# Performance work log

Measured on AMD Instinct MI355X. Metric: run time of the kernel, lower is better.

## Reference

```python
import jax, jax.numpy as jnp
import numpy as np

B, L, C, F, K = 16, 512, 384, 384, 3
MAX_DUR = 8
MEL_MAX = L * MAX_DUR  # fixed expanded length (padded/masked)
PAD = (K - 1) // 2


def conv1d(x, w, b):
    # x: [B, T, C] ; w: [F, C, K] ; 'same' padding as Conv1d(padding=(K-1)//2)
    y = jax.lax.conv_general_dilated(x.transpose(0, 2, 1), w, (1,), [(PAD, PAD)],
                                     dimension_numbers=('NCH', 'OIH', 'NCH'))
    return y.transpose(0, 2, 1) + b


def layernorm(x, g, b, eps=1e-5):
    mu = jnp.mean(x, axis=-1, keepdims=True)
    var = jnp.mean(jnp.square(x - mu), axis=-1, keepdims=True)
    return (x - mu) * jax.lax.rsqrt(var + eps) * g + b


def predictor(x, w1, b1, g1, be1, w2, b2, g2, be2, wl, bl):
    # Conv -> ReLU -> LN -> (Dropout=id) -> Conv -> ReLU -> LN -> Linear(F,1)
    h = layernorm(jax.nn.relu(conv1d(x, w1, b1)), g1, be1)
    h = layernorm(jax.nn.relu(conv1d(h, w2, b2)), g2, be2)
    return h @ wl + bl  # [B, T, 1]


def length_regulate(x, dur):
    # gather/repeat-interleave form of the dense one-hot alignment matmul
    cum = jnp.cumsum(dur, axis=-1)                       # [B, L]
    t = jnp.arange(MEL_MAX)                              # [T]
    idx = (t[None, :, None] >= cum[:, None, :]).sum(-1)  # [B, T] frame->phoneme
    idx = jnp.minimum(idx, x.shape[1] - 1)
    out = jnp.take_along_axis(x, idx[..., None], axis=1)  # [B, T, C]
    mask = (t[None, :] < cum[:, -1:]).astype(x.dtype)      # zero padded frames
    return out * mask[..., None]


def _pred_params(key, prefix):
    ks = jax.random.split(key, 4)
    s = 0.05
    return {
        f'{prefix}_w1': jax.random.normal(ks[0], (F, C, K), jnp.float32) * s,
        f'{prefix}_b1': jnp.zeros((F,), jnp.float32),
        f'{prefix}_g1': jnp.ones((F,), jnp.float32),
        f'{prefix}_be1': jnp.zeros((F,), jnp.float32),
        f'{prefix}_w2': jax.random.normal(ks[1], (F, F, K), jnp.float32) * s,
        f'{prefix}_b2': jnp.zeros((F,), jnp.float32),
        f'{prefix}_g2': jnp.ones((F,), jnp.float32),
        f'{prefix}_be2': jnp.zeros((F,), jnp.float32),
        f'{prefix}_wl': jax.random.normal(ks[2], (F, 1), jnp.float32) * s,
        f'{prefix}_bl': jnp.zeros((1,), jnp.float32),
    }


def setup_inputs() -> dict:
    key = jax.random.key(0)
    kx, kd, k1, k2, k3 = jax.random.split(key, 5)
    inp = {'x': jax.random.normal(kx, (B, L, C), jnp.float32)}
    inp.update(_pred_params(k1, 'dp'))
    inp.update(_pred_params(k2, 'pp'))
    inp.update(_pred_params(k3, 'ep'))
    inp['dur'] = jax.random.randint(kd, (B, L), 0, MAX_DUR, jnp.int32)
    return inp


def reference(x,
              dp_w1, dp_b1, dp_g1, dp_be1, dp_w2, dp_b2, dp_g2, dp_be2, dp_wl, dp_bl,
              pp_w1, pp_b1, pp_g1, pp_be1, pp_w2, pp_b2, pp_g2, pp_be2, pp_wl, pp_bl,
              ep_w1, ep_b1, ep_g1, ep_be1, ep_w2, ep_b2, ep_g2, ep_be2, ep_wl, ep_bl,
              dur):
    durations = predictor(x, dp_w1, dp_b1, dp_g1, dp_be1, dp_w2, dp_b2, dp_g2, dp_be2, dp_wl, dp_bl)
    expanded = length_regulate(x, dur)                    # [B, MEL_MAX, C]
    pitches = predictor(expanded, pp_w1, pp_b1, pp_g1, pp_be1, pp_w2, pp_b2, pp_g2, pp_be2, pp_wl, pp_bl)
    out = expanded + pitches
    energies = predictor(out, ep_w1, ep_b1, ep_g1, ep_be1, ep_w2, ep_b2, ep_g2, ep_be2, ep_wl, ep_bl)
    out = out + energies
    return (out, durations, pitches, energies)
```

## Files before the change

### kernel.cpp

```cpp
#include <hip/hip_runtime.h>
#include <stdint.h>
#include <stdio.h>

#define BB   16
#define LL   512
#define CC   384
#define FF   384
#define KW   3
#define MEL  4096
#define KKT  (CC*KW)

#define O_OUT 0
#define N_OUT (BB*MEL*CC)
#define O_DUR (N_OUT)
#define O_PIT (O_DUR + BB*LL)
#define O_EN  (O_PIT + BB*MEL)

using bf16x8 = __attribute__((ext_vector_type(8))) short;
using f32x4  = __attribute__((ext_vector_type(4))) float;

__device__ __forceinline__ unsigned short f2bf(float v) {
    union { float f; unsigned int u; } cv; cv.f = v;
    unsigned int u = cv.u;
    u += 0x7FFFu + ((u >> 16) & 1u);
    return (unsigned short)(u >> 16);
}
__device__ __forceinline__ float bf2f(unsigned short u) {
    union { unsigned int u; float f; } cv; cv.u = ((unsigned int)u) << 16; return cv.f;
}

__device__ __forceinline__ void gld_lds16(const unsigned short* gp, unsigned short* lp) {
    __builtin_amdgcn_global_load_lds(
        (const __attribute__((address_space(1))) unsigned int*)gp,
        (__attribute__((address_space(3))) unsigned int*)lp, 16, 0, 0);
}

__global__ void wtrans_kernel(const float* __restrict__ w, unsigned short* __restrict__ wt2) {
    int i = blockIdx.x * 256 + threadIdx.x;
    if (i >= FF * KKT) return;
    const int t = i / 24576;
    const int r = i - t * 24576;
    const int c = r >> 3;
    const int e = r & 7;
    const int q = c / 384;
    const int bn = c - q * 384;
    const int kk = t * 64 + q * 8 + e;
    const int k = kk / CC;
    const int ch = kk - k * CC;
    wt2[i] = f2bf(w[(size_t)bn * KKT + ch * KW + k]);
}

__global__ void convert_x_kernel(const float* __restrict__ x, unsigned short* __restrict__ o) {
    int i = blockIdx.x * 256 + threadIdx.x;
    if (i >= BB * LL * CC) return;
    int b = i / (LL * CC);
    int r = i - b * (LL * CC);
    int t = r / CC;
    int c = r - t * CC;
    o[((size_t)b * (LL + 2) + t + 1) * CC + c] = f2bf(x[i]);
}

__global__ void zpad_kernel(unsigned short* __restrict__ buf, int T) {
    int b = blockIdx.x >> 1;
    int w = blockIdx.x & 1;
    size_t row = (size_t)b * (T + 2) + (w ? (T + 1) : 0);
    buf[row * CC + threadIdx.x] = 0;
}

template<int T, bool FL>
__global__ __launch_bounds__(512)
void conv_ln_kernel(const unsigned short* __restrict__ inb,
                    const unsigned short* __restrict__ wt2,
                    const float* __restrict__ bias,
                    const float* __restrict__ g,
                    const float* __restrict__ be,
                    unsigned short* __restrict__ outb,
                    const float* __restrict__ wl,
                    const float* __restrict__ bl,
                    float* __restrict__ op) {
    __shared__ __align__(16) unsigned short LDS[4][8192];

    constexpr int NT = KKT / 64;
    const int m0 = blockIdx.x * 128;
    const int b  = m0 / T;
    const int t0 = m0 - b * T;
    const int tid  = threadIdx.x;
    const int lane = tid & 63;
    const int wv   = tid >> 6;
    const int wr   = wv >> 2;
    const int wc   = wv & 3;
    const int q0   = lane >> 4;
    const int l15  = lane & 15;

    const int rowS = tid >> 3;
    const int gch  = (tid & 7) ^ (rowS & 7);
    const unsigned short* srcA0 =
        inb + ((size_t)b * (T + 2) + t0 + rowS) * CC + gch * 8;
    const unsigned short* srcA1 =
        inb + ((size_t)b * (T + 2) + t0 + 64 + rowS) * CC + gch * 8;
    const unsigned short* wtb0 = wt2 + (size_t)((q0)     * 384 + wc * 96 + l15) * 8;
    const unsigned short* wtb1 = wt2 + (size_t)((4 + q0) * 384 + wc * 96 + l15) * 8;

    f32x4 acc[4][6] = {};
    bf16x8 bA[6], bB[6];

    auto stageA = [&](int bi, int t) {
        const int off = t * 64;
        gld_lds16(srcA0 + off, &LDS[bi][wv * 512]);
        gld_lds16(srcA1 + off, &LDS[bi][4096 + wv * 512]);
    };
    auto loadB0 = [&](int t) {
        const unsigned short* p = wtb0 + (size_t)t * 24576;
        #pragma unroll
        for (int j = 0; j < 6; ++j) bA[j] = *(const bf16x8*)(p + j * 128);
    };
    auto loadB1 = [&](int t) {
        const unsigned short* p = wtb1 + (size_t)t * 24576;
        #pragma unroll
        for (int j = 0; j < 6; ++j) bB[j] = *(const bf16x8*)(p + j * 128);
    };
    auto computeK = [&](int bi, int kkq, const bf16x8* br) {
        bf16x8 af[4];
        const int ca = kkq ^ (lane & 7);
        #pragma unroll
        for (int i = 0; i < 4; ++i) {
            const int ar = wr * 64 + i * 16 + l15;
            af[i] = *(const bf16x8*)(&LDS[bi][ar * 64 + ca * 8]);
        }
        __builtin_amdgcn_s_setprio(1);
        #pragma unroll
        for (int i = 0; i < 4; ++i)
            #pragma unroll
            for (int j = 0; j < 6; ++j)
                acc[i][j] = __builtin_amdgcn_mfma_f32_16x16x32_bf16(
                    af[i], br[j], acc[i][j], 0, 0, 0);
        __builtin_amdgcn_s_setprio(0);
    };

    stageA(0, 0);
    loadB0(0);
    stageA(1, 1);
    asm volatile("s_waitcnt vmcnt(8)" ::: "memory");

    for (int t = 0; t < NT; ++t) {
        __builtin_amdgcn_s_barrier();
        asm volatile("" ::: "memory");
        loadB1(t);
        stageA((t + 2) & 3, (t + 2 > NT - 1) ? NT - 1 : t + 2);
        asm volatile("s_waitcnt vmcnt(8)" ::: "memory");
        computeK(t & 3, q0, bA);
        loadB0((t + 1 > NT - 1) ? NT - 1 : t + 1);
        asm volatile("s_waitcnt vmcnt(8)" ::: "memory");
        computeK(t & 3, 4 + q0, bB);
    }
    asm volatile("s_waitcnt vmcnt(0)" ::: "memory");
    __syncthreads();

    const int colb = wc * 96 + (lane & 15);
    float b6[6];
    #pragma unroll
    for (int j = 0; j < 6; ++j) b6[j] = bias[colb + j * 16];
    #pragma unroll
    for (int i = 0; i < 4; ++i)
        #pragma unroll
        for (int j = 0; j < 6; ++j)
            #pragma unroll
            for (int r = 0; r < 4; ++r) {
                float v = acc[i][j][r] + b6[j];
                acc[i][j][r] = v > 0.f ? v : 0.f;
            }

    float S1[4][4], S2[4][4];
    #pragma unroll
    for (int i = 0; i < 4; ++i)
        #pragma unroll
        for (int r = 0; r < 4; ++r) {
            float s = 0.f, s2 = 0.f;
            #pragma unroll
            for (int j = 0; j < 6; ++j) { const float v = acc[i][j][r]; s += v; s2 += v * v; }
            #pragma unroll
            for (int m = 1; m <= 8; m <<= 1) { s += __shfl_xor(s, m); s2 += __shfl_xor(s2, m); }
            S1[i][r] = s; S2[i][r] = s2;
        }

    float2* red = (float2*)&LDS[0][0];
    if ((lane & 15) == 0) {
        const int q = lane >> 4;
        #pragma unroll
        for (int i = 0; i < 4; ++i)
            #pragma unroll
            for (int r = 0; r < 4; ++r)
                red[(wr * 64 + i * 16 + q * 4 + r) * 4 + wc] = make_float2(S1[i][r], S2[i][r]);
    }
    __syncthreads();

    float g6[6], be6[6];
    #pragma unroll
    for (int j = 0; j < 6; ++j) { g6[j] = g[colb + j * 16]; be6[j] = be[colb + j * 16]; }

    if (!FL) {
        #pragma unroll
        for (int i = 0; i < 4; ++i)
            #pragma unroll
            for (int r = 0; r < 4; ++r) {
                const int row = wr * 64 + i * 16 + (lane >> 4) * 4 + r;
                const float2 p0 = red[row * 4 + 0], p1 = red[row * 4 + 1];
                const float2 p2 = red[row * 4 + 2], p3 = red[row * 4 + 3];
                const float S = p0.x + p1.x + p2.x + p3.x;
                const float Q = p0.y + p1.y + p2.y + p3.y;
                const float mu = S * (1.f / 384.f);
                const float rs = rsqrtf(Q * (1.f / 384.f) - mu * mu + 1e-5f);
                unsigned short* qp = outb + ((size_t)b * (T + 2) + t0 + row + 1) * CC + colb;
                #pragma unroll
                for (int j = 0; j < 6; ++j)
                    qp[j * 16] = f2bf((acc[i][j][r] - mu) * rs * g6[j] + be6[j]);
            }
    } else {
        float wl6[6];
        #pragma unroll
        for (int j = 0; j < 6; ++j) wl6[j] = wl[colb + j * 16];
        float* redl = (float*)&LDS[1][0];
        #pragma unroll
        for (int i = 0; i < 4; ++i)
            #pragma unroll
            for (int r = 0; r < 4; ++r) {
                const int row = wr * 64 + i * 16 + (lane >> 4) * 4 + r;
                const float2 p0 = red[row * 4 + 0], p1 = red[row * 4 + 1];
                const float2 p2 = red[row * 4 + 2], p3 = red[row * 4 + 3];
                const float S = p0.x + p1.x + p2.x + p3.x;
                const float Q = p0.y + p1.y + p2.y + p3.y;
                const float mu = S * (1.f / 384.f);
                const float rs = rsqrtf(Q * (1.f / 384.f) - mu * mu + 1e-5f);
                float sl = 0.f;
                #pragma unroll
                for (int j = 0; j < 6; ++j)
                    sl += ((acc[i][j][r] - mu) * rs * g6[j] + be6[j]) * wl6[j];
                #pragma unroll
                for (int m = 1; m <= 8; m <<= 1) sl += __shfl_xor(sl, m);
                if ((lane & 15) == 0) redl[row * 4 + wc] = sl;
            }
        __syncthreads();
        if (tid < 128)
            op[m0 + tid] = redl[tid * 4] + redl[tid * 4 + 1] +
                           redl[tid * 4 + 2] + redl[tid * 4 + 3] + bl[0];
    }
}

__global__ void cumsum_kernel(const int* __restrict__ dur, int* __restrict__ cum) {
    __shared__ int s[LL];
    const int b = blockIdx.x, t = threadIdx.x;
    s[t] = dur[b * LL + t];
    __syncthreads();
    for (int off = 1; off < LL; off <<= 1) {
        int v = (t >= off) ? s[t - off] : 0;
        __syncthreads();
        s[t] += v;
        __syncthreads();
    }
    cum[b * LL + t] = s[t];
}

__global__ void idx_kernel(const int* __restrict__ cum, int* __restrict__ idxm) {
    const int i = blockIdx.x * 256 + threadIdx.x;
    if (i >= BB * MEL) return;
    const int b = i / MEL, t = i - b * MEL;
    const int* cb = cum + b * LL;
    const int total = cb[LL - 1];
    int lo = 0, hi = LL;
    while (lo < hi) {
        const int mid = (lo + hi) >> 1;
        if (cb[mid] <= t) lo = mid + 1; else hi = mid;
    }
    int id = lo > LL - 1 ? LL - 1 : lo;
    idxm[i] = (t < total) ? id : -1;
}

__global__ void gather_kernel(const float* __restrict__ x, const int* __restrict__ idxm,
                              unsigned short* __restrict__ bb0) {
    const int i = blockIdx.x * 256 + threadIdx.x;
    const int row = i / 96;
    const int c4  = (i - row * 96) * 4;
    const int b = row >> 12, t = row & (MEL - 1);
    const int id = idxm[row];
    float4 v = make_float4(0.f, 0.f, 0.f, 0.f);
    if (id >= 0) v = *(const float4*)(x + ((size_t)b * LL + id) * CC + c4);
    uint2 pk;
    pk.x = (unsigned int)f2bf(v.x) | ((unsigned int)f2bf(v.y) << 16);
    pk.y = (unsigned int)f2bf(v.z) | ((unsigned int)f2bf(v.w) << 16);
    *(uint2*)(bb0 + ((size_t)b * (MEL + 2) + t + 1) * CC + c4) = pk;
}

__global__ void addp_kernel(const unsigned short* __restrict__ bb0,
                            const float* __restrict__ pv,
                            unsigned short* __restrict__ be0) {
    const int i = blockIdx.x * 256 + threadIdx.x;
    const int row = i / 48;
    const int c8  = (i - row * 48) * 8;
    const int b = row >> 12, t = row & (MEL - 1);
    const float p = pv[row];
    const size_t o = ((size_t)b * (MEL + 2) + t + 1) * CC + c8;
    const uint4 in = *(const uint4*)(bb0 + o);
    uint4 ot;
    const unsigned int w[4] = {in.x, in.y, in.z, in.w};
    unsigned int r[4];
    #pragma unroll
    for (int k = 0; k < 4; ++k) {
        const float lo = bf2f((unsigned short)w[k]) + p;
        const float hi = bf2f((unsigned short)(w[k] >> 16)) + p;
        r[k] = (unsigned int)f2bf(lo) | ((unsigned int)f2bf(hi) << 16);
    }
    ot.x = r[0]; ot.y = r[1]; ot.z = r[2]; ot.w = r[3];
    *(uint4*)(be0 + o) = ot;
}

__global__ void final_kernel(const float* __restrict__ x, const int* __restrict__ idxm,
                             const float* __restrict__ pv, const float* __restrict__ ev,
                             float* __restrict__ out0) {
    const int i = blockIdx.x * 256 + threadIdx.x;
    const int row = i / 96;
    const int c4  = (i - row * 96) * 4;
    const int b = row >> 12;
    const int id = idxm[row];
    const float add = pv[row] + ev[row];
    float4 v = make_float4(0.f, 0.f, 0.f, 0.f);
    if (id >= 0) v = *(const float4*)(x + ((size_t)b * LL + id) * CC + c4);
    v.x += add; v.y += add; v.z += add; v.w += add;
    *(float4*)(out0 + (size_t)row * CC + c4) = v;
}

extern "C" void kernel_launch(void* const* d_in, const int* in_sizes, int n_in,
                              void* d_out, int out_size, void* d_ws, size_t ws_size,
                              hipStream_t stream) {
    const float* x = (const float*)d_in[0];
    const float* P[30];
    for (int i = 0; i < 30; ++i) P[i] = (const float*)d_in[1 + i];
    const int* dur = (const int*)d_in[31];
    float* out = (float*)d_out;

    char* ws = (char*)d_ws;
    const size_t WTT_ELEMS = (size_t)FF * KKT;
    const size_t WTT_BYTES = WTT_ELEMS * 2;
    unsigned short* wtt[6];
    for (int i = 0; i < 6; ++i) wtt[i] = (unsigned short*)(ws + i * WTT_BYTES);
    int* cum  = (int*)(ws + 5308416);
    int* idxm = (int*)(ws + 5341184);
    unsigned short* sb0 = (unsigned short*)(ws + 5603328);
    unsigned short* h1s = (unsigned short*)(ws + 11919360);
    unsigned short* bb0 = (unsigned short*)(ws + 18235392);
    unsigned short* h1p = (unsigned short*)(ws + 68616192);
    unsigned short* be0 = (unsigned short*)(ws + 118996992);
    const size_t need = 169377792;
    if (ws_size < need)
        fprintf(stderr, "kernel_launch: ws too small: %zu < %zu\n", ws_size, need);

    const float *dp_w1=P[0], *dp_b1=P[1], *dp_g1=P[2], *dp_be1=P[3], *dp_w2=P[4],
                *dp_b2=P[5], *dp_g2=P[6], *dp_be2=P[7], *dp_wl=P[8], *dp_bl=P[9];
    const float *pp_w1=P[10], *pp_b1=P[11], *pp_g1=P[12], *pp_be1=P[13], *pp_w2=P[14],
                *pp_b2=P[15], *pp_g2=P[16], *pp_be2=P[17], *pp_wl=P[18], *pp_bl=P[19];
    const float *ep_w1=P[20], *ep_b1=P[21], *ep_g1=P[22], *ep_be1=P[23], *ep_w2=P[24],
                *ep_b2=P[25], *ep_g2=P[26], *ep_be2=P[27], *ep_wl=P[28], *ep_bl=P[29];

    const int wtg = (int)((WTT_ELEMS + 255) / 256);
    wtrans_kernel<<<wtg, 256, 0, stream>>>(dp_w1, wtt[0]);
    wtrans_kernel<<<wtg, 256, 0, stream>>>(dp_w2, wtt[1]);
    wtrans_kernel<<<wtg, 256, 0, stream>>>(pp_w1, wtt[2]);
    wtrans_kernel<<<wtg, 256, 0, stream>>>(pp_w2, wtt[3]);
    wtrans_kernel<<<wtg, 256, 0, stream>>>(ep_w1, wtt[4]);
    wtrans_kernel<<<wtg, 256, 0, stream>>>(ep_w2, wtt[5]);

    convert_x_kernel<<<(BB * LL * CC + 255) / 256, 256, 0, stream>>>(x, sb0);
    zpad_kernel<<<BB * 2, CC, 0, stream>>>(sb0, LL);
    zpad_kernel<<<BB * 2, CC, 0, stream>>>(h1s, LL);
    zpad_kernel<<<BB * 2, CC, 0, stream>>>(bb0, MEL);
    zpad_kernel<<<BB * 2, CC, 0, stream>>>(h1p, MEL);
    zpad_kernel<<<BB * 2, CC, 0, stream>>>(be0, MEL);

    cumsum_kernel<<<BB, LL, 0, stream>>>(dur, cum);
    idx_kernel<<<(BB * MEL + 255) / 256, 256, 0, stream>>>(cum, idxm);

    conv_ln_kernel<LL, false><<<BB * LL / 128, 512, 0, stream>>>(
        sb0, wtt[0], dp_b1, dp_g1, dp_be1, h1s, nullptr, nullptr, nullptr);
    conv_ln_kernel<LL, true><<<BB * LL / 128, 512, 0, stream>>>(
        h1s, wtt[1], dp_b2, dp_g2, dp_be2, nullptr, dp_wl, dp_bl, out + O_DUR);

    gather_kernel<<<BB * MEL * 96 / 256, 256, 0, stream>>>(x, idxm, bb0);

    conv_ln_kernel<MEL, false><<<BB * MEL / 128, 512, 0, stream>>>(
        bb0, wtt[2], pp_b1, pp_g1, pp_be1, h1p, nullptr, nullptr, nullptr);
    conv_ln_kernel<MEL, true><<<BB * MEL / 128, 512, 0, stream>>>(
        h1p, wtt[3], pp_b2, pp_g2, pp_be2, nullptr, pp_wl, pp_bl, out + O_PIT);

    addp_kernel<<<BB * MEL * 48 / 256, 256, 0, stream>>>(bb0, out + O_PIT, be0);

    conv_ln_kernel<MEL, false><<<BB * MEL / 128, 512, 0, stream>>>(
        be0, wtt[4], ep_b1, ep_g1, ep_be1, h1p, nullptr, nullptr, nullptr);
    conv_ln_kernel<MEL, true><<<BB * MEL / 128, 512, 0, stream>>>(
        h1p, wtt[5], ep_b2, ep_g2, ep_be2, nullptr, ep_wl, ep_bl, out + O_EN);

    final_kernel<<<BB * MEL * 96 / 256, 256, 0, stream>>>(
        x, idxm, out + O_PIT, out + O_EN, out + O_OUT);
}
```

Baseline: 449.9 us.

## Repartition conv GEMM warps to full-row 128x48 tiles and unroll pipeline by two

Each of the 8 waves now covers all 128 rows of the block against 48 output columns, where before a 2x4 wave grid gave each wave 64 rows by 96 columns. The aim is to halve per-wave B-fragment global loads and register pressure. The cost is twice the LDS A-fragment reads per wave and an 8-way LayerNorm reduction instead of 4-way. The main loop is also manually unrolled by two with retuned vmcnt waits to overlap staging with MFMA. This unrolling assumes NT is even and relies on carefully counted wait thresholds.

```diff
diff --git a/kernel.cpp b/kernel.cpp
--- a/kernel.cpp
+++ b/kernel.cpp
@@ -87,8 +87,6 @@
     const int tid  = threadIdx.x;
     const int lane = tid & 63;
     const int wv   = tid >> 6;
-    const int wr   = wv >> 2;
-    const int wc   = wv & 3;
     const int q0   = lane >> 4;
     const int l15  = lane & 15;
 
@@ -98,11 +96,11 @@
         inb + ((size_t)b * (T + 2) + t0 + rowS) * CC + gch * 8;
     const unsigned short* srcA1 =
         inb + ((size_t)b * (T + 2) + t0 + 64 + rowS) * CC + gch * 8;
-    const unsigned short* wtb0 = wt2 + (size_t)((q0)     * 384 + wc * 96 + l15) * 8;
-    const unsigned short* wtb1 = wt2 + (size_t)((4 + q0) * 384 + wc * 96 + l15) * 8;
-
-    f32x4 acc[4][6] = {};
-    bf16x8 bA[6], bB[6];
+    const unsigned short* wtb0 = wt2 + (size_t)((q0)     * 384 + wv * 48 + l15) * 8;
+    const unsigned short* wtb1 = wt2 + (size_t)((4 + q0) * 384 + wv * 48 + l15) * 8;
+
+    f32x4 acc[8][3] = {};
+    bf16x8 bA[3], bB[3];
 
     auto stageA = [&](int bi, int t) {
         const int off = t * 64;
@@ -112,137 +110,144 @@
     auto loadB0 = [&](int t) {
         const unsigned short* p = wtb0 + (size_t)t * 24576;
         #pragma unroll
-        for (int j = 0; j < 6; ++j) bA[j] = *(const bf16x8*)(p + j * 128);
+        for (int j = 0; j < 3; ++j) bA[j] = *(const bf16x8*)(p + j * 128);
     };
     auto loadB1 = [&](int t) {
         const unsigned short* p = wtb1 + (size_t)t * 24576;
         #pragma unroll
-        for (int j = 0; j < 6; ++j) bB[j] = *(const bf16x8*)(p + j * 128);
+        for (int j = 0; j < 3; ++j) bB[j] = *(const bf16x8*)(p + j * 128);
     };
     auto computeK = [&](int bi, int kkq, const bf16x8* br) {
-        bf16x8 af[4];
-        const int ca = kkq ^ (lane & 7);
-        #pragma unroll
-        for (int i = 0; i < 4; ++i) {
-            const int ar = wr * 64 + i * 16 + l15;
+        bf16x8 af[8];
+        const int ca = kkq ^ (l15 & 7);
+        #pragma unroll
+        for (int i = 0; i < 8; ++i) {
+            const int ar = i * 16 + l15;
             af[i] = *(const bf16x8*)(&LDS[bi][ar * 64 + ca * 8]);
         }
         __builtin_amdgcn_s_setprio(1);
         #pragma unroll
-        for (int i = 0; i < 4; ++i)
-            #pragma unroll
-            for (int j = 0; j < 6; ++j)
+        for (int i = 0; i < 8; ++i)
+            #pragma unroll
+            for (int j = 0; j < 3; ++j)
                 acc[i][j] = __builtin_amdgcn_mfma_f32_16x16x32_bf16(
                     af[i], br[j], acc[i][j], 0, 0, 0);
         __builtin_amdgcn_s_setprio(0);
     };
 
     stageA(0, 0);
+    stageA(1, 1);
     loadB0(0);
-    stageA(1, 1);
-    asm volatile("s_waitcnt vmcnt(8)" ::: "memory");
-
-    for (int t = 0; t < NT; ++t) {
+    asm volatile("s_waitcnt vmcnt(3)" ::: "memory");
+
+    #pragma unroll 1
+    for (int t = 0; t < NT; t += 2) {
         __builtin_amdgcn_s_barrier();
         asm volatile("" ::: "memory");
+        stageA((t + 2) & 3, (t + 2 > NT - 1) ? NT - 1 : t + 2);
         loadB1(t);
-        stageA((t + 2) & 3, (t + 2 > NT - 1) ? NT - 1 : t + 2);
-        asm volatile("s_waitcnt vmcnt(8)" ::: "memory");
+        asm volatile("s_waitcnt vmcnt(5)" ::: "memory");
         computeK(t & 3, q0, bA);
-        loadB0((t + 1 > NT - 1) ? NT - 1 : t + 1);
-        asm volatile("s_waitcnt vmcnt(8)" ::: "memory");
+        loadB0(t + 1);
+        asm volatile("s_waitcnt vmcnt(3)" ::: "memory");
         computeK(t & 3, 4 + q0, bB);
+        stageA((t + 3) & 3, (t + 3 > NT - 1) ? NT - 1 : t + 3);
+        loadB1(t + 1);
+        asm volatile("s_waitcnt vmcnt(5)" ::: "memory");
+        computeK((t + 1) & 3, q0, bA);
+        loadB0((t + 2 > NT - 1) ? NT - 1 : t + 2);
+        asm volatile("s_waitcnt vmcnt(5)" ::: "memory");
+        computeK((t + 1) & 3, 4 + q0, bB);
+        asm volatile("s_waitcnt vmcnt(3)" ::: "memory");
     }
     asm volatile("s_waitcnt vmcnt(0)" ::: "memory");
     __syncthreads();
 
-    const int colb = wc * 96 + (lane & 15);
-    float b6[6];
+    const int colb = wv * 48 + l15;
+    float b3[3];
     #pragma unroll
-    for (int j = 0; j < 6; ++j) b6[j] = bias[colb + j * 16];
+    for (int j = 0; j < 3; ++j) b3[j] = bias[colb + j * 16];
     #pragma unroll
-    for (int i = 0; i < 4; ++i)
-        #pragma unroll
-        for (int j = 0; j < 6; ++j)
+    for (int i = 0; i < 8; ++i)
+        #pragma unroll
+        for (int j = 0; j < 3; ++j)
             #pragma unroll
             for (int r = 0; r < 4; ++r) {
-                float v = acc[i][j][r] + b6[j];
+                float v = acc[i][j][r] + b3[j];
                 acc[i][j][r] = v > 0.f ? v : 0.f;
             }
 
-    float S1[4][4], S2[4][4];
+    float2* red = (float2*)&LDS[0][0];
     #pragma unroll
-    for (int i = 0; i < 4; ++i)
+    for (int i = 0; i < 8; ++i)
         #pragma unroll
         for (int r = 0; r < 4; ++r) {
             float s = 0.f, s2 = 0.f;
             #pragma unroll
-            for (int j = 0; j < 6; ++j) { const float v = acc[i][j][r]; s += v; s2 += v * v; }
+            for (int j = 0; j < 3; ++j) { const float v = acc[i][j][r]; s += v; s2 += v * v; }
             #pragma unroll
             for (int m = 1; m <= 8; m <<= 1) { s += __shfl_xor(s, m); s2 += __shfl_xor(s2, m); }
-            S1[i][r] = s; S2[i][r] = s2;
+            if (l15 == 0)
+                red[(i * 16 + q0 * 4 + r) * 8 + wv] = make_float2(s, s2);
         }
-
-    float2* red = (float2*)&LDS[0][0];
-    if ((lane & 15) == 0) {
-        const int q = lane >> 4;
-        #pragma unroll
-        for (int i = 0; i < 4; ++i)
-            #pragma unroll
-            for (int r = 0; r < 4; ++r)
-                red[(wr * 64 + i * 16 + q * 4 + r) * 4 + wc] = make_float2(S1[i][r], S2[i][r]);
-    }
     __syncthreads();
 
-    float g6[6], be6[6];
+    float g3[3], be3[3];
     #pragma unroll
-    for (int j = 0; j < 6; ++j) { g6[j] = g[colb + j * 16]; be6[j] = be[colb + j * 16]; }
+    for (int j = 0; j < 3; ++j) { g3[j] = g[colb + j * 16]; be3[j] = be[colb + j * 16]; }
 
     if (!FL) {
         #pragma unroll
-        for (int i = 0; i < 4; ++i)
+        for (int i = 0; i < 8; ++i)
             #pragma unroll
             for (int r = 0; r < 4; ++r) {
-                const int row = wr * 64 + i * 16 + (lane >> 4) * 4 + r;
-                const float2 p0 = red[row * 4 + 0], p1 = red[row * 4 + 1];
-                const float2 p2 = red[row * 4 + 2], p3 = red[row * 4 + 3];
-                const float S = p0.x + p1.x + p2.x + p3.x;
-                const float Q = p0.y + p1.y + p2.y + p3.y;
+                const int row = i * 16 + q0 * 4 + r;
+                float S = 0.f, Q = 0.f;
+                #pragma unroll
+                for (int w = 0; w < 8; ++w) {
+                    const float2 p = red[row * 8 + w];
+                    S += p.x; Q += p.y;
+                }
                 const float mu = S * (1.f / 384.f);
                 const float rs = rsqrtf(Q * (1.f / 384.f) - mu * mu + 1e-5f);
                 unsigned short* qp = outb + ((size_t)b * (T + 2) + t0 + row + 1) * CC + colb;
                 #pragma unroll
-                for (int j = 0; j < 6; ++j)
-                    qp[j * 16] = f2bf((acc[i][j][r] - mu) * rs * g6[j] + be6[j]);
+                for (int j = 0; j < 3; ++j)
+                    qp[j * 16] = f2bf((acc[i][j][r] - mu) * rs * g3[j] + be3[j]);
             }
     } else {
-        float wl6[6];
-        #pragma unroll
-        for (int j = 0; j < 6; ++j) wl6[j] = wl[colb + j * 16];
+        float wl3[3];
+        #pragma unroll
+        for (int j = 0; j < 3; ++j) wl3[j] = wl[colb + j * 16];
         float* redl = (float*)&LDS[1][0];
         #pragma unroll
-        for (int i = 0; i < 4; ++i)
+        for (int i = 0; i < 8; ++i)
             #pragma unroll
             for (int r = 0; r < 4; ++r) {
-                const int row = wr * 64 + i * 16 + (lane >> 4) * 4 + r;
-                const float2 p0 = red[row * 4 + 0], p1 = red[row * 4 + 1];
-                const float2 p2 = red[row * 4 + 2], p3 = red[row * 4 + 3];
-                const float S = p0.x + p1.x + p2.x + p3.x;
-                const float Q = p0.y + p1.y + p2.y + p3.y;
+                const int row = i * 16 + q0 * 4 + r;
+                float S = 0.f, Q = 0.f;
+                #pragma unroll
+                for (int w = 0; w < 8; ++w) {
+                    const float2 p = red[row * 8 + w];
+                    S += p.x; Q += p.y;
+                }
                 const float mu = S * (1.f / 384.f);
                 const float rs = rsqrtf(Q * (1.f / 384.f) - mu * mu + 1e-5f);
                 float sl = 0.f;
                 #pragma unroll
-                for (int j = 0; j < 6; ++j)
-                    sl += ((acc[i][j][r] - mu) * rs * g6[j] + be6[j]) * wl6[j];
+                for (int j = 0; j < 3; ++j)
+                    sl += ((acc[i][j][r] - mu) * rs * g3[j] + be3[j]) * wl3[j];
                 #pragma unroll
                 for (int m = 1; m <= 8; m <<= 1) sl += __shfl_xor(sl, m);
-                if ((lane & 15) == 0) redl[row * 4 + wc] = sl;
+                if (l15 == 0) redl[row * 8 + wv] = sl;
             }
         __syncthreads();
-        if (tid < 128)
-            op[m0 + tid] = redl[tid * 4] + redl[tid * 4 + 1] +
-                           redl[tid * 4 + 2] + redl[tid * 4 + 3] + bl[0];
+        if (tid < 128) {
+            float s = bl[0];
+            #pragma unroll
+            for (int w = 0; w < 8; ++w) s += redl[tid * 8 + w];
+            op[m0 + tid] = s;
+        }
     }
 }
 
```

Result: slower. 461.3 us (+2.5%).

## Unroll conv main loop by two with double-buffered weight registers; bf16 final gather

Applied to the files above, without the earlier changes.

The conv+LayerNorm GEMM main loop now processes two K-tiles per iteration. It stages two A tiles into LDS at once, keeps two sets of B-fragment registers to prefetch weights one tile ahead, and drops the explicit vmcnt waits. It also hits the barrier only once per two tiles. The goal is to cut barrier and wait stalls and overlap more memory traffic with MFMA work, at the cost of extra registers and reliance on compiler-inserted waits for the direct-to-LDS loads. The final kernel now reads the already-expanded bf16 buffer instead of re-gathering fp32 x through the index map, which halves read traffic but rounds the residual path to bf16.

```diff
diff --git a/kernel.cpp b/kernel.cpp
--- a/kernel.cpp
+++ b/kernel.cpp
@@ -102,24 +102,19 @@
     const unsigned short* wtb1 = wt2 + (size_t)((4 + q0) * 384 + wc * 96 + l15) * 8;
 
     f32x4 acc[4][6] = {};
-    bf16x8 bA[6], bB[6];
+    bf16x8 bA0[6], bB0[6], bA1[6], bB1[6];
 
     auto stageA = [&](int bi, int t) {
         const int off = t * 64;
         gld_lds16(srcA0 + off, &LDS[bi][wv * 512]);
         gld_lds16(srcA1 + off, &LDS[bi][4096 + wv * 512]);
     };
-    auto loadB0 = [&](int t) {
-        const unsigned short* p = wtb0 + (size_t)t * 24576;
-        #pragma unroll
-        for (int j = 0; j < 6; ++j) bA[j] = *(const bf16x8*)(p + j * 128);
+    auto loadB = [&](bf16x8* d, const unsigned short* wb, int t) {
+        const unsigned short* p = wb + (size_t)t * 24576;
+        #pragma unroll
+        for (int j = 0; j < 6; ++j) d[j] = *(const bf16x8*)(p + j * 128);
     };
-    auto loadB1 = [&](int t) {
-        const unsigned short* p = wtb1 + (size_t)t * 24576;
-        #pragma unroll
-        for (int j = 0; j < 6; ++j) bB[j] = *(const bf16x8*)(p + j * 128);
-    };
-    auto computeK = [&](int bi, int kkq, const bf16x8* br) {
+    auto mfma24 = [&](int bi, int kkq, const bf16x8* br) {
         bf16x8 af[4];
         const int ca = kkq ^ (lane & 7);
         #pragma unroll
@@ -138,25 +133,34 @@
     };
 
     stageA(0, 0);
-    loadB0(0);
     stageA(1, 1);
-    asm volatile("s_waitcnt vmcnt(8)" ::: "memory");
-
-    for (int t = 0; t < NT; ++t) {
+    asm volatile("" ::: "memory");
+    loadB(bA0, wtb0, 0);
+    asm volatile("s_waitcnt vmcnt(6)" ::: "memory");
+
+    #pragma unroll 1
+    for (int t = 0; t < NT; t += 2) {
         __builtin_amdgcn_s_barrier();
         asm volatile("" ::: "memory");
-        loadB1(t);
-        stageA((t + 2) & 3, (t + 2 > NT - 1) ? NT - 1 : t + 2);
-        asm volatile("s_waitcnt vmcnt(8)" ::: "memory");
-        computeK(t & 3, q0, bA);
-        loadB0((t + 1 > NT - 1) ? NT - 1 : t + 1);
-        asm volatile("s_waitcnt vmcnt(8)" ::: "memory");
-        computeK(t & 3, 4 + q0, bB);
+        const int t2 = (t + 2 > NT - 1) ? NT - 1 : t + 2;
+        const int t3 = (t + 3 > NT - 1) ? NT - 1 : t + 3;
+        stageA((t + 2) & 3, t2);
+        stageA((t + 3) & 3, t3);
+        asm volatile("" ::: "memory");
+        loadB(bB0, wtb1, t);
+        loadB(bA1, wtb0, t + 1);
+        mfma24(t & 3, q0, bA0);
+        mfma24(t & 3, 4 + q0, bB0);
+        loadB(bB1, wtb1, t + 1);
+        mfma24((t + 1) & 3, q0, bA1);
+        loadB(bA0, wtb0, t2);
+        mfma24((t + 1) & 3, 4 + q0, bB1);
+        asm volatile("" ::: "memory");
     }
     asm volatile("s_waitcnt vmcnt(0)" ::: "memory");
     __syncthreads();
 
-    const int colb = wc * 96 + (lane & 15);
+    const int colb = wc * 96 + l15;
     float b6[6];
     #pragma unroll
     for (int j = 0; j < 6; ++j) b6[j] = bias[colb + j * 16];
@@ -184,13 +188,12 @@
         }
 
     float2* red = (float2*)&LDS[0][0];
-    if ((lane & 15) == 0) {
-        const int q = lane >> 4;
+    if (l15 == 0) {
         #pragma unroll
         for (int i = 0; i < 4; ++i)
             #pragma unroll
             for (int r = 0; r < 4; ++r)
-                red[(wr * 64 + i * 16 + q * 4 + r) * 4 + wc] = make_float2(S1[i][r], S2[i][r]);
+                red[(wr * 64 + i * 16 + q0 * 4 + r) * 4 + wc] = make_float2(S1[i][r], S2[i][r]);
     }
     __syncthreads();
 
@@ -203,7 +206,7 @@
         for (int i = 0; i < 4; ++i)
             #pragma unroll
             for (int r = 0; r < 4; ++r) {
-                const int row = wr * 64 + i * 16 + (lane >> 4) * 4 + r;
+                const int row = wr * 64 + i * 16 + q0 * 4 + r;
                 const float2 p0 = red[row * 4 + 0], p1 = red[row * 4 + 1];
                 const float2 p2 = red[row * 4 + 2], p3 = red[row * 4 + 3];
                 const float S = p0.x + p1.x + p2.x + p3.x;
@@ -219,12 +222,12 @@
         float wl6[6];
         #pragma unroll
         for (int j = 0; j < 6; ++j) wl6[j] = wl[colb + j * 16];
-        float* redl = (float*)&LDS[1][0];
+        float* redl = (float*)&LDS[2][0];
         #pragma unroll
         for (int i = 0; i < 4; ++i)
             #pragma unroll
             for (int r = 0; r < 4; ++r) {
-                const int row = wr * 64 + i * 16 + (lane >> 4) * 4 + r;
+                const int row = wr * 64 + i * 16 + q0 * 4 + r;
                 const float2 p0 = red[row * 4 + 0], p1 = red[row * 4 + 1];
                 const float2 p2 = red[row * 4 + 2], p3 = red[row * 4 + 3];
                 const float S = p0.x + p1.x + p2.x + p3.x;
@@ -237,7 +240,7 @@
                     sl += ((acc[i][j][r] - mu) * rs * g6[j] + be6[j]) * wl6[j];
                 #pragma unroll
                 for (int m = 1; m <= 8; m <<= 1) sl += __shfl_xor(sl, m);
-                if ((lane & 15) == 0) redl[row * 4 + wc] = sl;
+                if (l15 == 0) redl[row * 4 + wc] = sl;
             }
         __syncthreads();
         if (tid < 128)
@@ -313,19 +316,24 @@
     *(uint4*)(be0 + o) = ot;
 }
 
-__global__ void final_kernel(const float* __restrict__ x, const int* __restrict__ idxm,
+__global__ void final_kernel(const unsigned short* __restrict__ bb0,
                              const float* __restrict__ pv, const float* __restrict__ ev,
                              float* __restrict__ out0) {
     const int i = blockIdx.x * 256 + threadIdx.x;
-    const int row = i / 96;
-    const int c4  = (i - row * 96) * 4;
-    const int b = row >> 12;
-    const int id = idxm[row];
+    const int row = i / 48;
+    const int c8  = (i - row * 48) * 8;
+    const int b = row >> 12, t = row & (MEL - 1);
     const float add = pv[row] + ev[row];
-    float4 v = make_float4(0.f, 0.f, 0.f, 0.f);
-    if (id >= 0) v = *(const float4*)(x + ((size_t)b * LL + id) * CC + c4);
-    v.x += add; v.y += add; v.z += add; v.w += add;
-    *(float4*)(out0 + (size_t)row * CC + c4) = v;
+    const uint4 in = *(const uint4*)(bb0 + ((size_t)b * (MEL + 2) + t + 1) * CC + c8);
+    const unsigned int w[4] = {in.x, in.y, in.z, in.w};
+    float4 o0, o1;
+    o0.x = bf2f((unsigned short)w[0]) + add; o0.y = bf2f((unsigned short)(w[0] >> 16)) + add;
+    o0.z = bf2f((unsigned short)w[1]) + add; o0.w = bf2f((unsigned short)(w[1] >> 16)) + add;
+    o1.x = bf2f((unsigned short)w[2]) + add; o1.y = bf2f((unsigned short)(w[2] >> 16)) + add;
+    o1.z = bf2f((unsigned short)w[3]) + add; o1.w = bf2f((unsigned short)(w[3] >> 16)) + add;
+    float* op = out0 + (size_t)row * CC + c8;
+    *(float4*)op = o0;
+    *(float4*)(op + 4) = o1;
 }
 
 extern "C" void kernel_launch(void* const* d_in, const int* in_sizes, int n_in,
@@ -397,6 +405,6 @@
     conv_ln_kernel<MEL, true><<<BB * MEL / 128, 512, 0, stream>>>(
         h1p, wtt[5], ep_b2, ep_g2, ep_be2, nullptr, ep_wl, ep_bl, out + O_EN);
 
-    final_kernel<<<BB * MEL * 96 / 256, 256, 0, stream>>>(
-        x, idxm, out + O_PIT, out + O_EN, out + O_OUT);
-}
+    final_kernel<<<BB * MEL * 48 / 256, 256, 0, stream>>>(
+        bb0, out + O_PIT, out + O_EN, out + O_OUT);
+}
```

New measurement: 436.1 us. -3.1%, faster.
